# Performance work log

Hardware: AMD Instinct MI355X
Metric: run time of the kernel (lower is better)

## Reference

```python
import jax, jax.numpy as jnp
import numpy as np

N_MODULES = 8
AG_HIDDEN = 512
N_HID = 512
OUT_SIZE = 10
BATCH = 8192


def _state_mask(n_modules, n0, n1):
    # torch: eye(M).repeat_interleave(n0, 0).repeat_interleave(n1, 1)
    m = jnp.eye(n_modules, dtype=jnp.float32)
    return jnp.repeat(jnp.repeat(m, n0, axis=0), n1, axis=1)


def setup_inputs() -> dict:
    key = jax.random.key(0)
    ks = jax.random.split(key, 5)
    d_in = N_MODULES * AG_HIDDEN
    d_hid = N_MODULES * N_HID
    d_out = N_MODULES * OUT_SIZE
    s1 = 1.0 / np.sqrt(d_in)
    s2 = 1.0 / np.sqrt(d_hid)
    return {
        "x": jax.random.normal(ks[0], (BATCH, d_in), jnp.float32),
        "W1": jax.random.uniform(ks[1], (d_hid, d_in), jnp.float32, -s1, s1),
        "b1": jax.random.uniform(ks[2], (d_hid,), jnp.float32, -s1, s1),
        "W2": jax.random.uniform(ks[3], (d_out, d_hid), jnp.float32, -s2, s2),
        "b2": jax.random.uniform(ks[4], (d_out,), jnp.float32, -s2, s2),
    }


def reference(x, W1, b1, W2, b2):
    # block-diagonal masks (intra-module connectivity only)
    mask1 = _state_mask(N_MODULES, N_HID, AG_HIDDEN)   # [d_hid, d_in]
    mask2 = _state_mask(N_MODULES, OUT_SIZE, N_HID)    # [d_out, d_hid]
    h = jax.nn.relu(x @ (W1 * mask1).T + b1)           # [B, d_hid]
    y = h @ (W2 * mask2).T + b2                        # [B, d_out]
    # split(OUT_SIZE, -1) then stack on dim 1 == reshape to [B, n_modules, OUT_SIZE]
    return y.reshape(y.shape[0], N_MODULES, OUT_SIZE)
```

## Files before the change

### kernel.cpp

```cpp
#include <hip/hip_runtime.h>


#define NMOD 8
#define DIM 512
#define OSZ 10
#define BATCH 8192
#define D_IN 4096
#define D_OUT 80
#define BM 128
#define BN 256
#define BK 32
#define NK (DIM / BK)

#define ASTRIDE 40
#define HSTRIDE 264
#define A_SZ 5120
#define B_SZ 8192

#define LDSA_SZ 5120
#define LDSB_SZ 8192

#define VMCNT(n) asm volatile("s_waitcnt vmcnt(" #n ")" ::: "memory")
#define LGKM0()  asm volatile("s_waitcnt lgkmcnt(0)" ::: "memory")
#define MEMFENCE() asm volatile("" ::: "memory")

typedef __attribute__((ext_vector_type(8))) short short8;
typedef __attribute__((ext_vector_type(4))) float float4v;
typedef __attribute__((ext_vector_type(4))) unsigned int uint4v;

__device__ __forceinline__ unsigned short f2bf(float f) {
    unsigned int u = __builtin_bit_cast(unsigned int, f);
    u += 0x7fffu + ((u >> 16) & 1u);
    return (unsigned short)(u >> 16);
}

__device__ __forceinline__ short8 cvt8(float4 a, float4 b) {
    unsigned int u0, u1, u2, u3;
    asm("v_cvt_pk_bf16_f32 %0, %1, %2" : "=v"(u0) : "v"(a.x), "v"(a.y));
    asm("v_cvt_pk_bf16_f32 %0, %1, %2" : "=v"(u1) : "v"(a.z), "v"(a.w));
    asm("v_cvt_pk_bf16_f32 %0, %1, %2" : "=v"(u2) : "v"(b.x), "v"(b.y));
    asm("v_cvt_pk_bf16_f32 %0, %1, %2" : "=v"(u3) : "v"(b.z), "v"(b.w));
    uint4v u = {u0, u1, u2, u3};
    return __builtin_bit_cast(short8, u);
}

__global__ void init_out_kernel(const float* __restrict__ b2, float* __restrict__ out) {
    int idx = blockIdx.x * 256 + threadIdx.x;
    out[idx] = b2[idx % D_OUT];
}

__global__ void cvt_w_kernel(const float* __restrict__ W1, ushort* __restrict__ w1b) {
    int j = blockIdx.x * 256 + threadIdx.x;
    int mm = j >> 16, rem = j & 65535, r = rem >> 7, c4 = rem & 127;
    float4 v = *(const float4*)(W1 + (size_t)(mm * DIM + r) * D_IN + mm * DIM + c4 * 4);
    *(ushort4*)(w1b + (size_t)mm * DIM * DIM + r * DIM + c4 * 4) =
        make_ushort4(f2bf(v.x), f2bf(v.y), f2bf(v.z), f2bf(v.w));
}

__global__ __launch_bounds__(256, 2)
void fused_pipe(const float* __restrict__ x, const ushort* __restrict__ w1b,
                const float* __restrict__ b1, const float* __restrict__ W2,
                float* __restrict__ out) {
    __shared__ __attribute__((aligned(16))) ushort smem[26624];
    ushort* A0 = smem;
    ushort* A1 = smem + A_SZ;
    ushort* B0 = smem + 2 * A_SZ;
    ushort* B1 = smem + 2 * A_SZ + B_SZ;
    ushort* ldsH = smem;

    const int tid  = threadIdx.x;
    const int wave = tid >> 6;
    const int lane = tid & 63;
    const int r16  = lane & 15;
    const int kq   = lane >> 4;

    const int bid     = blockIdx.x;
    const int m       = bid & 7;
    const int half    = (bid >> 3) & 1;
    const int rowBase = (bid >> 4) * BM;

    const float*  xsrc = x + (size_t)rowBase * D_IN + m * DIM;
    const ushort* w1h  = w1b + (size_t)m * DIM * DIM + (size_t)half * BN * DIM;

    const int arow = tid >> 1;
    const int ah   = tid & 1;
    const int brow = tid >> 2;
    const int bc   = tid & 3;

    float4v acc[8][4];
#pragma unroll
    for (int i = 0; i < 8; i++)
#pragma unroll
        for (int j = 0; j < 4; j++) acc[i][j] = (float4v){0.f, 0.f, 0.f, 0.f};

    float4 xrA[4], xrB[4];

    auto issueX = [&](int k, float4 (&xr)[4]) {
        const float* p = xsrc + (size_t)arow * D_IN + k * BK + ah * 16;
        xr[0] = *(const float4*)p;       xr[1] = *(const float4*)(p + 4);
        xr[2] = *(const float4*)(p + 8); xr[3] = *(const float4*)(p + 12);
    };
    auto issueW = [&](int k, ushort* Bn) {
#pragma unroll
        for (int r = 0; r < 4; r++) {
            const int row = r * 64 + brow;
            const int f   = (row >> 1) & 3;
            __builtin_amdgcn_global_load_lds(
                (const __attribute__((address_space(1))) void*)(w1h + (size_t)row * DIM + k * BK + (bc ^ f) * 8),
                (__attribute__((address_space(3))) void*)(Bn + row * BK + bc * 8), 16, 0, 0);
        }
    };
    auto writeA = [&](float4 (&xr)[4], ushort* An) {
        *(short8*)(An + arow * ASTRIDE + ah * 16)     = cvt8(xr[0], xr[1]);
        *(short8*)(An + arow * ASTRIDE + ah * 16 + 8) = cvt8(xr[2], xr[3]);
    };
    auto compute = [&](const ushort* Ac, const ushort* Bc) {
        short8 aF[8], bF[4];
#pragma unroll
        for (int mt = 0; mt < 8; mt++)
            aF[mt] = *(const short8*)(Ac + (mt * 16 + r16) * ASTRIDE + kq * 8);
#pragma unroll
        for (int nt = 0; nt < 4; nt++) {
            const int row = wave * 64 + nt * 16 + r16;
            bF[nt] = *(const short8*)(Bc + row * BK + (kq ^ ((row >> 1) & 3)) * 8);
        }
#pragma unroll
        for (int mt = 0; mt < 8; mt++)
#pragma unroll
            for (int nt = 0; nt < 4; nt++)
                acc[mt][nt] = __builtin_amdgcn_mfma_f32_16x16x32_bf16(aF[mt], bF[nt], acc[mt][nt], 0, 0, 0);
    };

    issueX(0, xrA);  MEMFENCE();
    issueW(0, B0);   MEMFENCE();
    issueX(1, xrB);
    VMCNT(4);
    writeA(xrA, A0);
    LGKM0();
    __builtin_amdgcn_s_barrier();
    MEMFENCE();

    for (int k2 = 0; k2 < 14; k2 += 2) {
        {
            issueW(k2 + 1, B1);  MEMFENCE();
            issueX(k2 + 2, xrA); MEMFENCE();
            compute(A0, B0);
            MEMFENCE();
            VMCNT(4);
            writeA(xrB, A1);
            LGKM0();
            __builtin_amdgcn_s_barrier();
            MEMFENCE();
        }
        {
            issueW(k2 + 2, B0);  MEMFENCE();
            issueX(k2 + 3, xrB); MEMFENCE();
            compute(A1, B1);
            MEMFENCE();
            VMCNT(4);
            writeA(xrA, A0);
            LGKM0();
            __builtin_amdgcn_s_barrier();
            MEMFENCE();
        }
    }
    {
        issueW(15, B1);  MEMFENCE();
        compute(A0, B0);
        MEMFENCE();
        VMCNT(0);
        writeA(xrB, A1);
        LGKM0();
        __builtin_amdgcn_s_barrier();
        MEMFENCE();
    }
    {
        compute(A1, B1);
        MEMFENCE();
    }

    float b1v[4];
#pragma unroll
    for (int nt = 0; nt < 4; nt++)
        b1v[nt] = b1[m * DIM + half * BN + wave * 64 + nt * 16 + r16];

    for (int hh = 0; hh < 2; hh++) {
        __syncthreads();
#pragma unroll
        for (int mt2 = 0; mt2 < 4; mt2++) {
            const int mt = hh * 4 + mt2;
#pragma unroll
            for (int nt = 0; nt < 4; nt++) {
#pragma unroll
                for (int reg = 0; reg < 4; reg++) {
                    float v = acc[mt][nt][reg] + b1v[nt];
                    v = v > 0.f ? v : 0.f;
                    const int lr  = mt2 * 16 + kq * 4 + reg;
                    const int col = wave * 64 + nt * 16 + r16;
                    ldsH[lr * HSTRIDE + col] = f2bf(v);
                }
            }
        }
        __syncthreads();

        {
            float4v acc2 = (float4v){0.f, 0.f, 0.f, 0.f};
            const int hrow = wave * 16 + r16;
            const float* w2row = W2 + (size_t)(m * OSZ + r16) * D_IN + m * DIM + half * BN;
#pragma unroll
            for (int kc = 0; kc < BN / 32; kc++) {
                const int c = kc * 32 + kq * 8;
                short8 hA = *(const short8*)(ldsH + hrow * HSTRIDE + c);
                short8 wb = {0, 0, 0, 0, 0, 0, 0, 0};
                if (r16 < OSZ) {
                    const float* p = w2row + c;
                    wb = cvt8(*(const float4*)p, *(const float4*)(p + 4));
                }
                acc2 = __builtin_amdgcn_mfma_f32_16x16x32_bf16(hA, wb, acc2, 0, 0, 0);
            }
            if (r16 < OSZ) {
#pragma unroll
                for (int reg = 0; reg < 4; reg++) {
                    const int grow = rowBase + hh * 64 + wave * 16 + kq * 4 + reg;
                    atomicAdd(out + (size_t)grow * D_OUT + m * OSZ + r16, acc2[reg]);
                }
            }
        }
    }
}

template <bool WPRE>
__global__ __launch_bounds__(256, 2)
void fused_kernel(const float* __restrict__ x, const float* __restrict__ W1,
                  const ushort* __restrict__ w1b, const float* __restrict__ b1,
                  const float* __restrict__ W2, const float* __restrict__ b2,
                  float* __restrict__ out) {
    __shared__ __attribute__((aligned(16))) ushort smem[26624];
    ushort* ldsA0 = smem;
    ushort* ldsA1 = smem + LDSA_SZ;
    ushort* ldsB0 = smem + 2 * LDSA_SZ;
    ushort* ldsB1 = smem + 2 * LDSA_SZ + LDSB_SZ;
    ushort* ldsH  = smem;

    const int tid  = threadIdx.x;
    const int wave = tid >> 6;
    const int lane = tid & 63;
    const int r16  = lane & 15;
    const int kq   = lane >> 4;

    const int bid     = blockIdx.x;
    const int m       = bid & 7;
    const int half    = (bid >> 3) & 1;
    const int rowBase = (bid >> 4) * BM;

    const float*  xsrc = x + (size_t)rowBase * D_IN + m * DIM;
    const ushort* w1h  = w1b + (size_t)m * DIM * DIM + (size_t)half * BN * DIM;
    const float*  w1f  = W1 + (size_t)(m * DIM + half * BN) * D_IN + m * DIM;

    const int arow = tid >> 1;
    const int ah   = tid & 1;
    const int brow = tid >> 2;
    const int bc   = tid & 3;

    float4v acc[8][4];
#pragma unroll
    for (int i = 0; i < 8; i++)
#pragma unroll
        for (int j = 0; j < 4; j++) acc[i][j] = (float4v){0.f, 0.f, 0.f, 0.f};

    if (WPRE) {
#pragma unroll
        for (int r = 0; r < 4; r++) {
            const int row = r * 64 + brow;
            const int f   = (row >> 1) & 3;
            __builtin_amdgcn_global_load_lds(
                (const __attribute__((address_space(1))) void*)(w1h + (size_t)row * DIM + (bc ^ f) * 8),
                (__attribute__((address_space(3))) void*)(ldsB0 + row * BK + bc * 8), 16, 0, 0);
        }
    } else {
#pragma unroll
        for (int r = 0; r < 4; r++) {
            const int row = r * 64 + brow;
            const int f   = (row >> 1) & 3;
            const float* p = w1f + (size_t)row * D_IN + bc * 8;
            *(short8*)(ldsB0 + row * BK + (bc ^ f) * 8) = cvt8(*(const float4*)p, *(const float4*)(p + 4));
        }
    }
    {
        const float* p = xsrc + (size_t)arow * D_IN + ah * 16;
        float4 a0 = *(const float4*)p, a1 = *(const float4*)(p + 4);
        float4 a2 = *(const float4*)(p + 8), a3 = *(const float4*)(p + 12);
        *(short8*)(ldsA0 + arow * ASTRIDE + ah * 16)     = cvt8(a0, a1);
        *(short8*)(ldsA0 + arow * ASTRIDE + ah * 16 + 8) = cvt8(a2, a3);
    }

    for (int kk = 0; kk < DIM / BK; kk++) {
        __syncthreads();
        ushort* Ac = (kk & 1) ? ldsA1 : ldsA0;
        ushort* Bc = (kk & 1) ? ldsB1 : ldsB0;
        ushort* An = (kk & 1) ? ldsA0 : ldsA1;
        ushort* Bn = (kk & 1) ? ldsB0 : ldsB1;

        float4 xr0, xr1, xr2, xr3;
        const bool pf = (kk < DIM / BK - 1);
        if (pf) {
            const int k0n = (kk + 1) * BK;
            if (WPRE) {
#pragma unroll
                for (int r = 0; r < 4; r++) {
                    const int row = r * 64 + brow;
                    const int f   = (row >> 1) & 3;
                    __builtin_amdgcn_global_load_lds(
                        (const __attribute__((address_space(1))) void*)(w1h + (size_t)row * DIM + k0n + (bc ^ f) * 8),
                        (__attribute__((address_space(3))) void*)(Bn + row * BK + bc * 8), 16, 0, 0);
                }
            }
            const float* p = xsrc + (size_t)arow * D_IN + kk * BK + BK + ah * 16;
            xr0 = *(const float4*)p;     xr1 = *(const float4*)(p + 4);
            xr2 = *(const float4*)(p + 8); xr3 = *(const float4*)(p + 12);
        }

        short8 aF[8], bF[4];
#pragma unroll
        for (int mt = 0; mt < 8; mt++)
            aF[mt] = *(const short8*)(Ac + (mt * 16 + r16) * ASTRIDE + kq * 8);
#pragma unroll
        for (int nt = 0; nt < 4; nt++) {
            const int row = wave * 64 + nt * 16 + r16;
            bF[nt] = *(const short8*)(Bc + row * BK + (kq ^ ((row >> 1) & 3)) * 8);
        }
#pragma unroll
        for (int mt = 0; mt < 8; mt++)
#pragma unroll
            for (int nt = 0; nt < 4; nt++)
                acc[mt][nt] = __builtin_amdgcn_mfma_f32_16x16x32_bf16(aF[mt], bF[nt], acc[mt][nt], 0, 0, 0);

        if (pf) {
            *(short8*)(An + arow * ASTRIDE + ah * 16)     = cvt8(xr0, xr1);
            *(short8*)(An + arow * ASTRIDE + ah * 16 + 8) = cvt8(xr2, xr3);
            if (!WPRE) {
#pragma unroll
                for (int r = 0; r < 4; r++) {
                    const int row = r * 64 + brow;
                    const int f   = (row >> 1) & 3;
                    const float* p = w1f + (size_t)row * D_IN + kk * BK + BK + bc * 8;
                    *(short8*)(Bn + row * BK + (bc ^ f) * 8) = cvt8(*(const float4*)p, *(const float4*)(p + 4));
                }
            }
        }
    }

    float b1v[4];
#pragma unroll
    for (int nt = 0; nt < 4; nt++)
        b1v[nt] = b1[m * DIM + half * BN + wave * 64 + nt * 16 + r16];

    for (int hh = 0; hh < 2; hh++) {
        __syncthreads();
#pragma unroll
        for (int mt2 = 0; mt2 < 4; mt2++) {
            const int mt = hh * 4 + mt2;
#pragma unroll
            for (int nt = 0; nt < 4; nt++) {
#pragma unroll
                for (int reg = 0; reg < 4; reg++) {
                    float v = acc[mt][nt][reg] + b1v[nt];
                    v = v > 0.f ? v : 0.f;
                    const int lr  = mt2 * 16 + kq * 4 + reg;
                    const int col = wave * 64 + nt * 16 + r16;
                    ldsH[lr * HSTRIDE + col] = f2bf(v);
                }
            }
        }
        __syncthreads();

        {
            float4v acc2 = (float4v){0.f, 0.f, 0.f, 0.f};
            const int hrow = wave * 16 + r16;
            const float* w2row = W2 + (size_t)(m * OSZ + r16) * D_IN + m * DIM + half * BN;
#pragma unroll
            for (int kc = 0; kc < BN / 32; kc++) {
                const int c = kc * 32 + kq * 8;
                short8 hA = *(const short8*)(ldsH + hrow * HSTRIDE + c);
                short8 wb = {0, 0, 0, 0, 0, 0, 0, 0};
                if (r16 < OSZ) {
                    const float* p = w2row + c;
                    wb = cvt8(*(const float4*)p, *(const float4*)(p + 4));
                }
                acc2 = __builtin_amdgcn_mfma_f32_16x16x32_bf16(hA, wb, acc2, 0, 0, 0);
            }
            if (r16 < OSZ) {
#pragma unroll
                for (int reg = 0; reg < 4; reg++) {
                    const int grow = rowBase + hh * 64 + wave * 16 + kq * 4 + reg;
                    atomicAdd(out + (size_t)grow * D_OUT + m * OSZ + r16, acc2[reg]);
                }
            }
        }
    }
}

extern "C" void kernel_launch(void* const* d_in, const int* in_sizes, int n_in,
                              void* d_out, int out_size, void* d_ws, size_t ws_size,
                              hipStream_t stream) {
    const float* x  = (const float*)d_in[0];
    const float* W1 = (const float*)d_in[1];
    const float* b1 = (const float*)d_in[2];
    const float* W2 = (const float*)d_in[3];
    const float* b2 = (const float*)d_in[4];
    float* out = (float*)d_out;

    init_out_kernel<<<dim3(2560), dim3(256), 0, stream>>>(b2, out);

    if (ws_size >= (size_t)NMOD * DIM * DIM * sizeof(ushort)) {
        ushort* w1b = (ushort*)d_ws;
        cvt_w_kernel<<<dim3(2048), dim3(256), 0, stream>>>(W1, w1b);
        fused_pipe<<<dim3(1024), dim3(256), 0, stream>>>(x, w1b, b1, W2, out);
    } else {
        fused_kernel<false><<<dim3(1024), dim3(256), 0, stream>>>(x, W1, nullptr, b1, W2, b2, out);
    }
}
```

Baseline: 258.3 us.

## Split hidden dimension into quarter tiles with 2x2 wave layout, raise occupancy

Each block of the fused pipelined kernel now computes a 128x128 hidden tile instead of 128x256, and the grid doubles to 2048 blocks. The four waves are arranged 2x2 over rows and columns, with smaller accumulators, W1 LDS buffers and H staging, and launch bounds raised to 3 blocks per CU. The aim is more parallelism and occupancy to hide memory latency. In exchange, each x tile is loaded and converted to bf16 four times instead of twice, and the number of output atomics doubles.

```diff
diff --git a/kernel.cpp b/kernel.cpp
--- a/kernel.cpp
+++ b/kernel.cpp
@@ -8,14 +8,14 @@
 #define D_IN 4096
 #define D_OUT 80
 #define BM 128
-#define BN 256
+#define BNQ 128
 #define BK 32
 #define NK (DIM / BK)
 
 #define ASTRIDE 40
-#define HSTRIDE 264
+#define HSTRIDE 136
 #define A_SZ 5120
-#define B_SZ 8192
+#define B_SZ 4096
 
 #define LDSA_SZ 5120
 #define LDSB_SZ 8192
@@ -57,11 +57,11 @@
         make_ushort4(f2bf(v.x), f2bf(v.y), f2bf(v.z), f2bf(v.w));
 }
 
-__global__ __launch_bounds__(256, 2)
+__global__ __launch_bounds__(256, 3)
 void fused_pipe(const float* __restrict__ x, const ushort* __restrict__ w1b,
                 const float* __restrict__ b1, const float* __restrict__ W2,
                 float* __restrict__ out) {
-    __shared__ __attribute__((aligned(16))) ushort smem[26624];
+    __shared__ __attribute__((aligned(16))) ushort smem[18432];
     ushort* A0 = smem;
     ushort* A1 = smem + A_SZ;
     ushort* B0 = smem + 2 * A_SZ;
@@ -73,23 +73,25 @@
     const int lane = tid & 63;
     const int r16  = lane & 15;
     const int kq   = lane >> 4;
+    const int wr   = wave >> 1;
+    const int wc   = wave & 1;
 
     const int bid     = blockIdx.x;
     const int m       = bid & 7;
-    const int half    = (bid >> 3) & 1;
-    const int rowBase = (bid >> 4) * BM;
+    const int q       = (bid >> 3) & 3;
+    const int rowBase = (bid >> 5) * BM;
 
     const float*  xsrc = x + (size_t)rowBase * D_IN + m * DIM;
-    const ushort* w1h  = w1b + (size_t)m * DIM * DIM + (size_t)half * BN * DIM;
+    const ushort* w1q  = w1b + (size_t)m * DIM * DIM + (size_t)q * BNQ * DIM;
 
     const int arow = tid >> 1;
     const int ah   = tid & 1;
     const int brow = tid >> 2;
     const int bc   = tid & 3;
 
-    float4v acc[8][4];
-#pragma unroll
-    for (int i = 0; i < 8; i++)
+    float4v acc[4][4];
+#pragma unroll
+    for (int i = 0; i < 4; i++)
 #pragma unroll
         for (int j = 0; j < 4; j++) acc[i][j] = (float4v){0.f, 0.f, 0.f, 0.f};
 
@@ -102,11 +104,11 @@
     };
     auto issueW = [&](int k, ushort* Bn) {
 #pragma unroll
-        for (int r = 0; r < 4; r++) {
+        for (int r = 0; r < 2; r++) {
             const int row = r * 64 + brow;
             const int f   = (row >> 1) & 3;
             __builtin_amdgcn_global_load_lds(
-                (const __attribute__((address_space(1))) void*)(w1h + (size_t)row * DIM + k * BK + (bc ^ f) * 8),
+                (const __attribute__((address_space(1))) void*)(w1q + (size_t)row * DIM + k * BK + (bc ^ f) * 8),
                 (__attribute__((address_space(3))) void*)(Bn + row * BK + bc * 8), 16, 0, 0);
         }
     };
@@ -115,17 +117,17 @@
         *(short8*)(An + arow * ASTRIDE + ah * 16 + 8) = cvt8(xr[2], xr[3]);
     };
     auto compute = [&](const ushort* Ac, const ushort* Bc) {
-        short8 aF[8], bF[4];
-#pragma unroll
-        for (int mt = 0; mt < 8; mt++)
-            aF[mt] = *(const short8*)(Ac + (mt * 16 + r16) * ASTRIDE + kq * 8);
+        short8 aF[4], bF[4];
+#pragma unroll
+        for (int mt = 0; mt < 4; mt++)
+            aF[mt] = *(const short8*)(Ac + (wr * 64 + mt * 16 + r16) * ASTRIDE + kq * 8);
 #pragma unroll
         for (int nt = 0; nt < 4; nt++) {
-            const int row = wave * 64 + nt * 16 + r16;
+            const int row = wc * 64 + nt * 16 + r16;
             bF[nt] = *(const short8*)(Bc + row * BK + (kq ^ ((row >> 1) & 3)) * 8);
         }
 #pragma unroll
-        for (int mt = 0; mt < 8; mt++)
+        for (int mt = 0; mt < 4; mt++)
 #pragma unroll
             for (int nt = 0; nt < 4; nt++)
                 acc[mt][nt] = __builtin_amdgcn_mfma_f32_16x16x32_bf16(aF[mt], bF[nt], acc[mt][nt], 0, 0, 0);
@@ -182,22 +184,23 @@
     float b1v[4];
 #pragma unroll
     for (int nt = 0; nt < 4; nt++)
-        b1v[nt] = b1[m * DIM + half * BN + wave * 64 + nt * 16 + r16];
+        b1v[nt] = b1[m * DIM + q * BNQ + wc * 64 + nt * 16 + r16];
 
     for (int hh = 0; hh < 2; hh++) {
         __syncthreads();
-#pragma unroll
-        for (int mt2 = 0; mt2 < 4; mt2++) {
-            const int mt = hh * 4 + mt2;
-#pragma unroll
-            for (int nt = 0; nt < 4; nt++) {
-#pragma unroll
-                for (int reg = 0; reg < 4; reg++) {
-                    float v = acc[mt][nt][reg] + b1v[nt];
-                    v = v > 0.f ? v : 0.f;
-                    const int lr  = mt2 * 16 + kq * 4 + reg;
-                    const int col = wave * 64 + nt * 16 + r16;
-                    ldsH[lr * HSTRIDE + col] = f2bf(v);
+        if (wr == hh) {
+#pragma unroll
+            for (int mt = 0; mt < 4; mt++) {
+#pragma unroll
+                for (int nt = 0; nt < 4; nt++) {
+#pragma unroll
+                    for (int reg = 0; reg < 4; reg++) {
+                        float v = acc[mt][nt][reg] + b1v[nt];
+                        v = v > 0.f ? v : 0.f;
+                        const int lr  = mt * 16 + kq * 4 + reg;
+                        const int col = wc * 64 + nt * 16 + r16;
+                        ldsH[lr * HSTRIDE + col] = f2bf(v);
+                    }
                 }
             }
         }
@@ -206,9 +209,9 @@
         {
             float4v acc2 = (float4v){0.f, 0.f, 0.f, 0.f};
             const int hrow = wave * 16 + r16;
-            const float* w2row = W2 + (size_t)(m * OSZ + r16) * D_IN + m * DIM + half * BN;
-#pragma unroll
-            for (int kc = 0; kc < BN / 32; kc++) {
+            const float* w2row = W2 + (size_t)(m * OSZ + r16) * D_IN + m * DIM + q * BNQ;
+#pragma unroll
+            for (int kc = 0; kc < BNQ / 32; kc++) {
                 const int c = kc * 32 + kq * 8;
                 short8 hA = *(const short8*)(ldsH + hrow * HSTRIDE + c);
                 short8 wb = {0, 0, 0, 0, 0, 0, 0, 0};
@@ -254,8 +257,8 @@
     const int rowBase = (bid >> 4) * BM;
 
     const float*  xsrc = x + (size_t)rowBase * D_IN + m * DIM;
-    const ushort* w1h  = w1b + (size_t)m * DIM * DIM + (size_t)half * BN * DIM;
-    const float*  w1f  = W1 + (size_t)(m * DIM + half * BN) * D_IN + m * DIM;
+    const ushort* w1h  = w1b + (size_t)m * DIM * DIM + (size_t)half * 256 * DIM;
+    const float*  w1f  = W1 + (size_t)(m * DIM + half * 256) * D_IN + m * DIM;
 
     const int arow = tid >> 1;
     const int ah   = tid & 1;
@@ -353,7 +356,7 @@
     float b1v[4];
 #pragma unroll
     for (int nt = 0; nt < 4; nt++)
-        b1v[nt] = b1[m * DIM + half * BN + wave * 64 + nt * 16 + r16];
+        b1v[nt] = b1[m * DIM + half * 256 + wave * 64 + nt * 16 + r16];
 
     for (int hh = 0; hh < 2; hh++) {
         __syncthreads();
@@ -368,7 +371,7 @@
                     v = v > 0.f ? v : 0.f;
                     const int lr  = mt2 * 16 + kq * 4 + reg;
                     const int col = wave * 64 + nt * 16 + r16;
-                    ldsH[lr * HSTRIDE + col] = f2bf(v);
+                    ldsH[lr * 264 + col] = f2bf(v);
                 }
             }
         }
@@ -377,11 +380,11 @@
         {
             float4v acc2 = (float4v){0.f, 0.f, 0.f, 0.f};
             const int hrow = wave * 16 + r16;
-            const float* w2row = W2 + (size_t)(m * OSZ + r16) * D_IN + m * DIM + half * BN;
-#pragma unroll
-            for (int kc = 0; kc < BN / 32; kc++) {
+            const float* w2row = W2 + (size_t)(m * OSZ + r16) * D_IN + m * DIM + half * 256;
+#pragma unroll
+            for (int kc = 0; kc < 256 / 32; kc++) {
                 const int c = kc * 32 + kq * 8;
-                short8 hA = *(const short8*)(ldsH + hrow * HSTRIDE + c);
+                short8 hA = *(const short8*)(ldsH + hrow * 264 + c);
                 short8 wb = {0, 0, 0, 0, 0, 0, 0, 0};
                 if (r16 < OSZ) {
                     const float* p = w2row + c;
@@ -415,7 +418,7 @@
     if (ws_size >= (size_t)NMOD * DIM * DIM * sizeof(ushort)) {
         ushort* w1b = (ushort*)d_ws;
         cvt_w_kernel<<<dim3(2048), dim3(256), 0, stream>>>(W1, w1b);
-        fused_pipe<<<dim3(1024), dim3(256), 0, stream>>>(x, w1b, b1, W2, out);
+        fused_pipe<<<dim3(2048), dim3(256), 0, stream>>>(x, w1b, b1, W2, out);
     } else {
         fused_kernel<false><<<dim3(1024), dim3(256), 0, stream>>>(x, W1, nullptr, b1, W2, b2, out);
     }
```

Result: slower. 271.6 us (+5.1%).

## Split GEMM k-step into two MFMA halves with barriers and raised priority

Applied to the files above, without the earlier changes.

Each k-step's compute is split into two halves, each doing the A-fragment LDS reads and then 16 MFMAs. Extra barriers are placed between the halves, and the MFMA blocks are wrapped in s_setprio(1). The aim is a ping-pong style schedule where waves alternate between memory/LDS phases and MFMA phases, so math overlaps better with global loads and LDS writes. It adds four barriers per k-step and changes vmcnt waits, which costs synchronisation overhead and risks stalls if the waves do not stagger as intended.

```diff
diff --git a/kernel.cpp b/kernel.cpp
--- a/kernel.cpp
+++ b/kernel.cpp
@@ -23,6 +23,7 @@
 #define VMCNT(n) asm volatile("s_waitcnt vmcnt(" #n ")" ::: "memory")
 #define LGKM0()  asm volatile("s_waitcnt lgkmcnt(0)" ::: "memory")
 #define MEMFENCE() asm volatile("" ::: "memory")
+#define BARRIER() do { __builtin_amdgcn_s_barrier(); MEMFENCE(); } while (0)
 
 typedef __attribute__((ext_vector_type(8))) short short8;
 typedef __attribute__((ext_vector_type(4))) float float4v;
@@ -114,21 +115,42 @@
         *(short8*)(An + arow * ASTRIDE + ah * 16)     = cvt8(xr[0], xr[1]);
         *(short8*)(An + arow * ASTRIDE + ah * 16 + 8) = cvt8(xr[2], xr[3]);
     };
-    auto compute = [&](const ushort* Ac, const ushort* Bc) {
-        short8 aF[8], bF[4];
-#pragma unroll
-        for (int mt = 0; mt < 8; mt++)
+
+    short8 aF[8], bF[4];
+    auto readA03 = [&](const ushort* Ac) {
+#pragma unroll
+        for (int mt = 0; mt < 4; mt++)
             aF[mt] = *(const short8*)(Ac + (mt * 16 + r16) * ASTRIDE + kq * 8);
+    };
+    auto readA47 = [&](const ushort* Ac) {
+#pragma unroll
+        for (int mt = 4; mt < 8; mt++)
+            aF[mt] = *(const short8*)(Ac + (mt * 16 + r16) * ASTRIDE + kq * 8);
+    };
+    auto readB = [&](const ushort* Bc) {
 #pragma unroll
         for (int nt = 0; nt < 4; nt++) {
             const int row = wave * 64 + nt * 16 + r16;
             bF[nt] = *(const short8*)(Bc + row * BK + (kq ^ ((row >> 1) & 3)) * 8);
         }
-#pragma unroll
-        for (int mt = 0; mt < 8; mt++)
+    };
+    auto mfma03 = [&]() {
+        __builtin_amdgcn_s_setprio(1);
+#pragma unroll
+        for (int mt = 0; mt < 4; mt++)
 #pragma unroll
             for (int nt = 0; nt < 4; nt++)
                 acc[mt][nt] = __builtin_amdgcn_mfma_f32_16x16x32_bf16(aF[mt], bF[nt], acc[mt][nt], 0, 0, 0);
+        __builtin_amdgcn_s_setprio(0);
+    };
+    auto mfma47 = [&]() {
+        __builtin_amdgcn_s_setprio(1);
+#pragma unroll
+        for (int mt = 4; mt < 8; mt++)
+#pragma unroll
+            for (int nt = 0; nt < 4; nt++)
+                acc[mt][nt] = __builtin_amdgcn_mfma_f32_16x16x32_bf16(aF[mt], bF[nt], acc[mt][nt], 0, 0, 0);
+        __builtin_amdgcn_s_setprio(0);
     };
 
     issueX(0, xrA);  MEMFENCE();
@@ -137,47 +159,64 @@
     VMCNT(4);
     writeA(xrA, A0);
     LGKM0();
-    __builtin_amdgcn_s_barrier();
-    MEMFENCE();
+    BARRIER();
+
+#define STEADY_ITER(KP1, KP2, Ac, Bc, An, Bn, XRD, XRI)                        \
+    do {                                                                       \
+        issueW((KP1), (Bn));  MEMFENCE();                                      \
+        issueX((KP2), (XRI)); MEMFENCE();                                      \
+        readA03((Ac)); readB((Bc));                                            \
+        LGKM0();                                                               \
+        BARRIER();                                                             \
+        mfma03();                                                              \
+        BARRIER();                                                             \
+        VMCNT(8);                                                              \
+        writeA((XRD), (An));                                                   \
+        readA47((Ac));                                                         \
+        LGKM0();                                                               \
+        BARRIER();                                                             \
+        mfma47();                                                              \
+        VMCNT(4);                                                              \
+        BARRIER();                                                             \
+    } while (0)
 
     for (int k2 = 0; k2 < 14; k2 += 2) {
-        {
-            issueW(k2 + 1, B1);  MEMFENCE();
-            issueX(k2 + 2, xrA); MEMFENCE();
-            compute(A0, B0);
-            MEMFENCE();
-            VMCNT(4);
-            writeA(xrB, A1);
-            LGKM0();
-            __builtin_amdgcn_s_barrier();
-            MEMFENCE();
-        }
-        {
-            issueW(k2 + 2, B0);  MEMFENCE();
-            issueX(k2 + 3, xrB); MEMFENCE();
-            compute(A1, B1);
-            MEMFENCE();
-            VMCNT(4);
-            writeA(xrA, A0);
-            LGKM0();
-            __builtin_amdgcn_s_barrier();
-            MEMFENCE();
-        }
+        STEADY_ITER(k2 + 1, k2 + 2, A0, B0, A1, B1, xrB, xrA);
+        if (k2 < 12) {
+            STEADY_ITER(k2 + 2, k2 + 3, A1, B1, A0, B0, xrA, xrB);
+        }
+    }
+    {
+        STEADY_ITER(14, 15, A1, B1, A0, B0, xrA, xrB);
     }
     {
         issueW(15, B1);  MEMFENCE();
-        compute(A0, B0);
-        MEMFENCE();
+        readA03(A0); readB(B0);
+        LGKM0();
+        BARRIER();
+        mfma03();
+        BARRIER();
+        VMCNT(4);
+        writeA(xrB, A1);
+        readA47(A0);
+        LGKM0();
+        BARRIER();
+        mfma47();
         VMCNT(0);
-        writeA(xrB, A1);
+        BARRIER();
+    }
+    {
+        readA03(A1); readB(B1);
         LGKM0();
-        __builtin_amdgcn_s_barrier();
-        MEMFENCE();
-    }
-    {
-        compute(A1, B1);
-        MEMFENCE();
-    }
+        BARRIER();
+        mfma03();
+        BARRIER();
+        readA47(A1);
+        LGKM0();
+        BARRIER();
+        mfma47();
+    }
+#undef STEADY_ITER
 
     float b1v[4];
 #pragma unroll
```

After: 258.9 us. No clear change (+0.2%).

## Deepen W1 prefetch pipeline and give each wave its own B rows

Applied to the files above, without the earlier changes.

Restructures the main loop of the fused GEMM so that W1 tiles are prefetched two k-steps ahead. The B tile's LDS buffer is refilled right after its fragments are read into registers, which lets the global-to-LDS load overlap the MFMAs. The W load mapping changes so each wave loads exactly the B rows it later reads. This removes the need for a cross-wave barrier before B is consumed, and waits are handled per wave with vmcnt. The fallback fused_kernel drops its unused template branch. The deeper pipeline adds more in-flight loads and depends on vmcnt counts being precise, so a wrong count could read stale data.

```diff
diff --git a/kernel.cpp b/kernel.cpp
--- a/kernel.cpp
+++ b/kernel.cpp
@@ -34,13 +34,14 @@
     return (unsigned short)(u >> 16);
 }
 
+__device__ __forceinline__ unsigned int pk2(float a, float b) {
+    unsigned int r;
+    asm("v_cvt_pk_bf16_f32 %0, %1, %2" : "=v"(r) : "v"(a), "v"(b));
+    return r;
+}
+
 __device__ __forceinline__ short8 cvt8(float4 a, float4 b) {
-    unsigned int u0, u1, u2, u3;
-    asm("v_cvt_pk_bf16_f32 %0, %1, %2" : "=v"(u0) : "v"(a.x), "v"(a.y));
-    asm("v_cvt_pk_bf16_f32 %0, %1, %2" : "=v"(u1) : "v"(a.z), "v"(a.w));
-    asm("v_cvt_pk_bf16_f32 %0, %1, %2" : "=v"(u2) : "v"(b.x), "v"(b.y));
-    asm("v_cvt_pk_bf16_f32 %0, %1, %2" : "=v"(u3) : "v"(b.z), "v"(b.w));
-    uint4v u = {u0, u1, u2, u3};
+    uint4v u = {pk2(a.x, a.y), pk2(a.z, a.w), pk2(b.x, b.y), pk2(b.z, b.w)};
     return __builtin_bit_cast(short8, u);
 }
 
@@ -84,8 +85,8 @@
 
     const int arow = tid >> 1;
     const int ah   = tid & 1;
-    const int brow = tid >> 2;
-    const int bc   = tid & 3;
+    const int bl4  = lane >> 2;
+    const int bc   = lane & 3;
 
     float4v acc[8][4];
 #pragma unroll
@@ -103,7 +104,7 @@
     auto issueW = [&](int k, ushort* Bn) {
 #pragma unroll
         for (int r = 0; r < 4; r++) {
-            const int row = r * 64 + brow;
+            const int row = wave * 64 + r * 16 + bl4;
             const int f   = (row >> 1) & 3;
             __builtin_amdgcn_global_load_lds(
                 (const __attribute__((address_space(1))) void*)(w1h + (size_t)row * DIM + k * BK + (bc ^ f) * 8),
@@ -114,16 +115,21 @@
         *(short8*)(An + arow * ASTRIDE + ah * 16)     = cvt8(xr[0], xr[1]);
         *(short8*)(An + arow * ASTRIDE + ah * 16 + 8) = cvt8(xr[2], xr[3]);
     };
-    auto compute = [&](const ushort* Ac, const ushort* Bc) {
-        short8 aF[8], bF[4];
+
+    short8 aF[8], bF[4];
+    auto readA = [&](const ushort* Ac) {
 #pragma unroll
         for (int mt = 0; mt < 8; mt++)
             aF[mt] = *(const short8*)(Ac + (mt * 16 + r16) * ASTRIDE + kq * 8);
+    };
+    auto readB = [&](const ushort* Bc) {
 #pragma unroll
         for (int nt = 0; nt < 4; nt++) {
             const int row = wave * 64 + nt * 16 + r16;
             bF[nt] = *(const short8*)(Bc + row * BK + (kq ^ ((row >> 1) & 3)) * 8);
         }
+    };
+    auto mfma = [&]() {
 #pragma unroll
         for (int mt = 0; mt < 8; mt++)
 #pragma unroll
@@ -133,49 +139,55 @@
 
     issueX(0, xrA);  MEMFENCE();
     issueW(0, B0);   MEMFENCE();
-    issueX(1, xrB);
-    VMCNT(4);
+    issueX(1, xrB);  MEMFENCE();
+    issueW(1, B1);
+    VMCNT(12);
     writeA(xrA, A0);
     LGKM0();
     __builtin_amdgcn_s_barrier();
     MEMFENCE();
 
+#define STEADY_ITER(KP2, Ac, Bc, An, XRD, XRI)                                 \
+    do {                                                                       \
+        issueX((KP2), (XRI)); MEMFENCE();                                      \
+        readA((Ac));                                                           \
+        VMCNT(12);                                                             \
+        readB((Bc));                                                           \
+        LGKM0();                                                               \
+        issueW((KP2), (Bc)); MEMFENCE();                                       \
+        mfma();                                                                \
+        MEMFENCE();                                                            \
+        VMCNT(12);                                                             \
+        writeA((XRD), (An));                                                   \
+        LGKM0();                                                               \
+        __builtin_amdgcn_s_barrier();                                          \
+        MEMFENCE();                                                            \
+    } while (0)
+
     for (int k2 = 0; k2 < 14; k2 += 2) {
-        {
-            issueW(k2 + 1, B1);  MEMFENCE();
-            issueX(k2 + 2, xrA); MEMFENCE();
-            compute(A0, B0);
-            MEMFENCE();
-            VMCNT(4);
-            writeA(xrB, A1);
-            LGKM0();
-            __builtin_amdgcn_s_barrier();
-            MEMFENCE();
-        }
-        {
-            issueW(k2 + 2, B0);  MEMFENCE();
-            issueX(k2 + 3, xrB); MEMFENCE();
-            compute(A1, B1);
-            MEMFENCE();
-            VMCNT(4);
-            writeA(xrA, A0);
-            LGKM0();
-            __builtin_amdgcn_s_barrier();
-            MEMFENCE();
-        }
-    }
+        STEADY_ITER(k2 + 2, A0, B0, A1, xrB, xrA);
+        STEADY_ITER(k2 + 3, A1, B1, A0, xrA, xrB);
+    }
+#undef STEADY_ITER
     {
-        issueW(15, B1);  MEMFENCE();
-        compute(A0, B0);
+        readA(A0);
+        VMCNT(8);
+        readB(B0);
+        LGKM0();
+        mfma();
         MEMFENCE();
-        VMCNT(0);
+        VMCNT(4);
         writeA(xrB, A1);
         LGKM0();
         __builtin_amdgcn_s_barrier();
         MEMFENCE();
     }
     {
-        compute(A1, B1);
+        readA(A1);
+        VMCNT(0);
+        readB(B1);
+        LGKM0();
+        mfma();
         MEMFENCE();
     }
 
@@ -229,11 +241,9 @@
     }
 }
 
-template <bool WPRE>
 __global__ __launch_bounds__(256, 2)
 void fused_kernel(const float* __restrict__ x, const float* __restrict__ W1,
-                  const ushort* __restrict__ w1b, const float* __restrict__ b1,
-                  const float* __restrict__ W2, const float* __restrict__ b2,
+                  const float* __restrict__ b1, const float* __restrict__ W2,
                   float* __restrict__ out) {
     __shared__ __attribute__((aligned(16))) ushort smem[26624];
     ushort* ldsA0 = smem;
@@ -254,7 +264,6 @@
     const int rowBase = (bid >> 4) * BM;
 
     const float*  xsrc = x + (size_t)rowBase * D_IN + m * DIM;
-    const ushort* w1h  = w1b + (size_t)m * DIM * DIM + (size_t)half * BN * DIM;
     const float*  w1f  = W1 + (size_t)(m * DIM + half * BN) * D_IN + m * DIM;
 
     const int arow = tid >> 1;
@@ -268,23 +277,12 @@
 #pragma unroll
         for (int j = 0; j < 4; j++) acc[i][j] = (float4v){0.f, 0.f, 0.f, 0.f};
 
-    if (WPRE) {
-#pragma unroll
-        for (int r = 0; r < 4; r++) {
-            const int row = r * 64 + brow;
-            const int f   = (row >> 1) & 3;
-            __builtin_amdgcn_global_load_lds(
-                (const __attribute__((address_space(1))) void*)(w1h + (size_t)row * DIM + (bc ^ f) * 8),
-                (__attribute__((address_space(3))) void*)(ldsB0 + row * BK + bc * 8), 16, 0, 0);
-        }
-    } else {
-#pragma unroll
-        for (int r = 0; r < 4; r++) {
-            const int row = r * 64 + brow;
-            const int f   = (row >> 1) & 3;
-            const float* p = w1f + (size_t)row * D_IN + bc * 8;
-            *(short8*)(ldsB0 + row * BK + (bc ^ f) * 8) = cvt8(*(const float4*)p, *(const float4*)(p + 4));
-        }
+#pragma unroll
+    for (int r = 0; r < 4; r++) {
+        const int row = r * 64 + brow;
+        const int f   = (row >> 1) & 3;
+        const float* p = w1f + (size_t)row * D_IN + bc * 8;
+        *(short8*)(ldsB0 + row * BK + (bc ^ f) * 8) = cvt8(*(const float4*)p, *(const float4*)(p + 4));
     }
     {
         const float* p = xsrc + (size_t)arow * D_IN + ah * 16;
@@ -294,7 +292,7 @@
         *(short8*)(ldsA0 + arow * ASTRIDE + ah * 16 + 8) = cvt8(a2, a3);
     }
 
-    for (int kk = 0; kk < DIM / BK; kk++) {
+    for (int kk = 0; kk < NK; kk++) {
         __syncthreads();
         ushort* Ac = (kk & 1) ? ldsA1 : ldsA0;
         ushort* Bc = (kk & 1) ? ldsB1 : ldsB0;
@@ -302,19 +300,8 @@
         ushort* Bn = (kk & 1) ? ldsB0 : ldsB1;
 
         float4 xr0, xr1, xr2, xr3;
-        const bool pf = (kk < DIM / BK - 1);
+        const bool pf = (kk < NK - 1);
         if (pf) {
-            const int k0n = (kk + 1) * BK;
-            if (WPRE) {
-#pragma unroll
-                for (int r = 0; r < 4; r++) {
-                    const int row = r * 64 + brow;
-                    const int f   = (row >> 1) & 3;
-                    __builtin_amdgcn_global_load_lds(
-                        (const __attribute__((address_space(1))) void*)(w1h + (size_t)row * DIM + k0n + (bc ^ f) * 8),
-                        (__attribute__((address_space(3))) void*)(Bn + row * BK + bc * 8), 16, 0, 0);
-                }
-            }
             const float* p = xsrc + (size_t)arow * D_IN + kk * BK + BK + ah * 16;
             xr0 = *(const float4*)p;     xr1 = *(const float4*)(p + 4);
             xr2 = *(const float4*)(p + 8); xr3 = *(const float4*)(p + 12);
@@ -338,14 +325,12 @@
         if (pf) {
             *(short8*)(An + arow * ASTRIDE + ah * 16)     = cvt8(xr0, xr1);
             *(short8*)(An + arow * ASTRIDE + ah * 16 + 8) = cvt8(xr2, xr3);
-            if (!WPRE) {
-#pragma unroll
-                for (int r = 0; r < 4; r++) {
-                    const int row = r * 64 + brow;
-                    const int f   = (row >> 1) & 3;
-                    const float* p = w1f + (size_t)row * D_IN + kk * BK + BK + bc * 8;
-                    *(short8*)(Bn + row * BK + (bc ^ f) * 8) = cvt8(*(const float4*)p, *(const float4*)(p + 4));
-                }
+#pragma unroll
+            for (int r = 0; r < 4; r++) {
+                const int row = r * 64 + brow;
+                const int f   = (row >> 1) & 3;
+                const float* p = w1f + (size_t)row * D_IN + kk * BK + BK + bc * 8;
+                *(short8*)(Bn + row * BK + (bc ^ f) * 8) = cvt8(*(const float4*)p, *(const float4*)(p + 4));
             }
         }
     }
@@ -417,6 +402,6 @@
         cvt_w_kernel<<<dim3(2048), dim3(256), 0, stream>>>(W1, w1b);
         fused_pipe<<<dim3(1024), dim3(256), 0, stream>>>(x, w1b, b1, W2, out);
     } else {
-        fused_kernel<false><<<dim3(1024), dim3(256), 0, stream>>>(x, W1, nullptr, b1, W2, b2, out);
-    }
-}
+        fused_kernel<<<dim3(1024), dim3(256), 0, stream>>>(x, W1, b1, W2, out);
+    }
+}
```

Measured after the change: 257.0 us. No clear change (-0.5%).
